# Kernel tuning notes

Measured on AMD Instinct MI355X. Metric: run time of the kernel, lower is better.

The kernel has to match this reference:

```python
import jax, jax.numpy as jnp
import numpy as np

N_HEADS = 16


def setup_inputs() -> dict:
    key = jax.random.key(0)
    ks = jax.random.split(key, 8)
    ts, td, b, hc = 64, 4096, 8, 1024
    scale = 1.0 / np.sqrt(hc)
    return {
        "s": jax.random.normal(ks[0], (ts, b, hc), dtype=jnp.float32),
        "d": jax.random.normal(ks[1], (td, b, hc), dtype=jnp.float32),
        "Wq": jax.random.normal(ks[2], (hc, hc), dtype=jnp.float32) * scale,
        "bq": jax.random.normal(ks[3], (hc,), dtype=jnp.float32) * 0.01,
        "Wk": jax.random.normal(ks[4], (hc, hc), dtype=jnp.float32) * scale,
        "bk": jax.random.normal(ks[5], (hc,), dtype=jnp.float32) * 0.01,
        "Wv": jax.random.normal(ks[6], (hc, hc), dtype=jnp.float32) * scale,
        "bv": jax.random.normal(ks[7], (hc,), dtype=jnp.float32) * 0.01,
    }


def reference(s, d, Wq, bq, Wk, bk, Wv, bv):
    ts, b, hc = s.shape
    td = d.shape[0]
    h = N_HEADS
    c = hc // h
    # linear projections (torch Linear: x @ W.T + b)
    q = (s @ Wq.T + bq).reshape(ts, b, h, c)
    k = (d @ Wk.T + bk).reshape(td, b, h, c)
    v = (d @ Wv.T + bv).reshape(td, b, h, c)
    # scores over (slot, token) pairs, scaled
    a = jnp.einsum('sbhc,dbhc->sdbh', q, k) / jnp.sqrt(jnp.asarray(c, s.dtype))
    # competitive softmax across the SLOT axis (dim 0), not the key axis
    a = jax.nn.softmax(a, axis=0)          # (ts, td, b, h)
    n = jnp.sum(a, axis=1) + 0.001         # (ts, b, h)
    num = jnp.einsum('sdbh,dbhc->sbhc', a, v)
    out = num / n[..., None]               # normalized weighted average
    return out.reshape(ts, b, hc)
```

## Files before the change

kernel.cpp:

```cpp
#include <hip/hip_runtime.h>


#define TS 64
#define TD 4096
#define BATCH 8
#define HC 1024
#define NHEAD 16
#define MD (TD*BATCH)
#define MS (TS*BATCH)
#define NCHUNK 8
#define CHTOK (TD/NCHUNK)

typedef __attribute__((ext_vector_type(8))) __bf16 bf16x8;
typedef __attribute__((ext_vector_type(4))) float f32x4;
typedef __attribute__((ext_vector_type(4))) unsigned short u16x4;
typedef __attribute__((ext_vector_type(8))) unsigned short u16x8;

__device__ __forceinline__ unsigned short f2bf(float x){
  union { float f; unsigned u; } v; v.f = x;
  unsigned r = v.u + 0x7FFFu + ((v.u >> 16) & 1u);
  return (unsigned short)(r >> 16);
}

__device__ __forceinline__ void gll16(const void* g, void* l){
  __builtin_amdgcn_global_load_lds((__attribute__((address_space(1))) void*)g,
                                   (__attribute__((address_space(3))) void*)l, 16, 0, 0);
}

__global__ void cvt_bf16(const float* __restrict__ in, unsigned short* __restrict__ out, int n4){
  int i = blockIdx.x * blockDim.x + threadIdx.x;
  if (i >= n4) return;
  f32x4 f = ((const f32x4*)in)[i];
  u16x4 o;
  o[0] = f2bf(f[0]); o[1] = f2bf(f[1]); o[2] = f2bf(f[2]); o[3] = f2bf(f[3]);
  ((u16x4*)out)[i] = o;
}

__global__ __launch_bounds__(256) void gemm128(
    const unsigned short* __restrict__ A,
    const unsigned short* __restrict__ W,
    const float* __restrict__ bias,
    unsigned short* __restrict__ C)
{
  __shared__ unsigned short As[128*64];
  __shared__ unsigned short Bs[128*64];
  const int nwg = gridDim.x;
  const int cpx = nwg >> 3;
  const int orig = blockIdx.x;
  const int wg = (orig & 7) * cpx + (orig >> 3);
  const int mt = wg >> 3, nt = wg & 7;
  const int tid = threadIdx.x;
  const int lane = tid & 63, w = tid >> 6;
  const int l15 = lane & 15, lg = lane >> 4;
  const int wr = w >> 1, wc = w & 1;

  const int lrow = lane >> 3;
  const int lch  = (lane & 7) << 4;
  const char* pA[4]; const char* pB[4]; unsigned ldsoff[4];
  #pragma unroll
  for (int j = 0; j < 4; ++j){
    int row = w*32 + j*8 + lrow;
    int sw  = lch ^ ((row & 7) << 4);
    pA[j] = (const char*)A + (size_t)(mt*128 + row) * 2048 + sw;
    pB[j] = (const char*)W + (size_t)(nt*128 + row) * 2048 + sw;
    ldsoff[j] = (unsigned)(w*32 + j*8) * 128;
  }

  const f32x4 fz = {0.f, 0.f, 0.f, 0.f};
  f32x4 acc[4][4];
  #pragma unroll
  for (int m = 0; m < 4; ++m)
    #pragma unroll
    for (int n = 0; n < 4; ++n) acc[m][n] = fz;

  for (int kt = 0; kt < 16; ++kt){
    __syncthreads();
    #pragma unroll
    for (int j = 0; j < 4; ++j){
      gll16(pA[j] + (size_t)kt*128, (char*)As + ldsoff[j]);
      gll16(pB[j] + (size_t)kt*128, (char*)Bs + ldsoff[j]);
    }
    __syncthreads();
    #pragma unroll
    for (int kk = 0; kk < 2; ++kk){
      bf16x8 af[4], bfr[4];
      #pragma unroll
      for (int m = 0; m < 4; ++m){
        int row = wr*64 + m*16 + l15;
        af[m] = *(const bf16x8*)((const char*)As + row*128 + ((lg*16 + kk*64) ^ ((row & 7) << 4)));
      }
      #pragma unroll
      for (int n = 0; n < 4; ++n){
        int row = wc*64 + n*16 + l15;
        bfr[n] = *(const bf16x8*)((const char*)Bs + row*128 + ((lg*16 + kk*64) ^ ((row & 7) << 4)));
      }
      #pragma unroll
      for (int m = 0; m < 4; ++m)
        #pragma unroll
        for (int n = 0; n < 4; ++n)
          acc[m][n] = __builtin_amdgcn_mfma_f32_16x16x32_bf16(af[m], bfr[n], acc[m][n], 0, 0, 0);
    }
  }

  const int ccol0 = nt*128 + wc*64;
  float bv[4];
  #pragma unroll
  for (int n = 0; n < 4; ++n) bv[n] = bias[ccol0 + n*16 + l15];
  #pragma unroll
  for (int m = 0; m < 4; ++m){
    #pragma unroll
    for (int r = 0; r < 4; ++r){
      size_t row = (size_t)(mt*128 + wr*64 + m*16 + lg*4 + r);
      unsigned short* cp = C + row*1024 + ccol0;
      #pragma unroll
      for (int n = 0; n < 4; ++n)
        cp[n*16 + l15] = f2bf(acc[m][n][r] + bv[n]);
    }
  }
}

__global__ __launch_bounds__(256) void attn_kernel(
    const unsigned short* __restrict__ Q,
    const unsigned short* __restrict__ K,
    const unsigned short* __restrict__ V,
    float* __restrict__ P)
{
  __shared__ unsigned short Qs[64*64];
  __shared__ unsigned short Ks[64*64];
  __shared__ unsigned short Vt[80*64];
  __shared__ unsigned short Al[64*64];
  __shared__ float red[256];

  const int bh = blockIdx.x;
  const int chunk = blockIdx.y;
  const int bb = bh >> 4, h = bh & 15;
  const int tid = threadIdx.x;
  const int lane = tid & 63, w = tid >> 6;
  const int l15 = lane & 15, lg = lane >> 4;
  const int lrow = lane >> 3, lch = (lane & 7) << 4;

  for (int i = tid; i < 16*64; i += 256){
    int r = i >> 6;
    Vt[(64 + r)*64 + (i & 63)] = (r == 0) ? (unsigned short)0x3F80 : (unsigned short)0;
  }

  #pragma unroll
  for (int j = 0; j < 2; ++j){
    int row = w*16 + j*8 + lrow;
    int sw = lch ^ ((row & 7) << 4);
    const char* g = (const char*)Q + (size_t)(row*BATCH + bb)*2048 + h*128 + sw;
    gll16(g, (char*)Qs + (w*16 + j*8)*128);
  }

  const f32x4 fz = {0.f, 0.f, 0.f, 0.f};
  f32x4 acc[5];
  #pragma unroll
  for (int nb = 0; nb < 5; ++nb) acc[nb] = fz;

  const int vtok = tid >> 2;
  const int vcg  = tid & 3;
  const int t0 = chunk * CHTOK;

  for (int tt = 0; tt < CHTOK/64; ++tt){
    const int tb = t0 + tt*64;
    #pragma unroll
    for (int j = 0; j < 2; ++j){
      int row = w*16 + j*8 + lrow;
      int sw = lch ^ ((row & 7) << 4);
      const char* g = (const char*)K + (size_t)((size_t)(tb + row)*BATCH + bb)*2048 + h*128 + sw;
      gll16(g, (char*)Ks + (w*16 + j*8)*128);
    }
    const char* vg = (const char*)V + (size_t)((size_t)(tb + vtok)*BATCH + bb)*2048 + h*128 + vcg*32;
    u16x8 v0 = *(const u16x8*)vg;
    u16x8 v1 = *(const u16x8*)(vg + 16);
    __syncthreads();

    bf16x8 qa[2];
    #pragma unroll
    for (int kk = 0; kk < 2; ++kk){
      int row = w*16 + l15;
      qa[kk] = *(const bf16x8*)((const char*)Qs + row*128 + ((lg*16 + kk*64) ^ ((row & 7) << 4)));
    }
    float e[4][4];
    #pragma unroll
    for (int nb = 0; nb < 4; ++nb){
      f32x4 s = fz;
      #pragma unroll
      for (int kk = 0; kk < 2; ++kk){
        int row = nb*16 + l15;
        bf16x8 kb = *(const bf16x8*)((const char*)Ks + row*128 + ((lg*16 + kk*64) ^ ((row & 7) << 4)));
        s = __builtin_amdgcn_mfma_f32_16x16x32_bf16(qa[kk], kb, s, 0, 0, 0);
      }
      #pragma unroll
      for (int r = 0; r < 4; ++r) e[nb][r] = __expf(s[r] * 0.125f);
    }
    #pragma unroll
    for (int nb = 0; nb < 4; ++nb){
      float cp = e[nb][0] + e[nb][1] + e[nb][2] + e[nb][3];
      cp += __shfl_xor(cp, 16);
      cp += __shfl_xor(cp, 32);
      if (lg == 0) red[w*64 + nb*16 + l15] = cp;
    }
    __syncthreads();

    #pragma unroll
    for (int nb = 0; nb < 4; ++nb){
      int col = nb*16 + l15;
      float dn = red[col] + red[64 + col] + red[128 + col] + red[192 + col];
      float inv = 1.0f / dn;
      #pragma unroll
      for (int r = 0; r < 4; ++r){
        int row = w*16 + lg*4 + r;
        Al[row*64 + ((((2*col)) ^ ((row & 7) << 4)) >> 1)] = f2bf(e[nb][r] * inv);
      }
    }
    #pragma unroll
    for (int ee = 0; ee < 8; ++ee){
      int c0 = vcg*16 + ee;
      int sw0 = (((c0 & 7) ^ (c0 >> 3)) & 7) << 4;
      Vt[c0*64 + (((2*vtok) ^ sw0) >> 1)] = v0[ee];
    }
    #pragma unroll
    for (int ee = 0; ee < 8; ++ee){
      int c1 = vcg*16 + 8 + ee;
      int sw1 = (((c1 & 7) ^ (c1 >> 3)) & 7) << 4;
      Vt[c1*64 + (((2*vtok) ^ sw1) >> 1)] = v1[ee];
    }
    __syncthreads();

    bf16x8 aa[2];
    #pragma unroll
    for (int kk = 0; kk < 2; ++kk){
      int row = w*16 + l15;
      aa[kk] = *(const bf16x8*)((const char*)Al + row*128 + ((lg*16 + kk*64) ^ ((row & 7) << 4)));
    }
    #pragma unroll
    for (int nb = 0; nb < 5; ++nb){
      #pragma unroll
      for (int kk = 0; kk < 2; ++kk){
        int row = nb*16 + l15;
        int sw = (((row & 7) ^ (row >> 3)) & 7) << 4;
        bf16x8 vb = *(const bf16x8*)((const char*)Vt + row*128 + ((lg*16 + kk*64) ^ sw));
        acc[nb] = __builtin_amdgcn_mfma_f32_16x16x32_bf16(aa[kk], vb, acc[nb], 0, 0, 0);
      }
    }
  }

  float* Pb = P + (size_t)(bh*NCHUNK + chunk) * 64 * 80;
  #pragma unroll
  for (int nb = 0; nb < 5; ++nb){
    #pragma unroll
    for (int r = 0; r < 4; ++r){
      int s = w*16 + lg*4 + r;
      Pb[(size_t)s*80 + nb*16 + l15] = acc[nb][r];
    }
  }
}

__global__ void reduce_out(const float* __restrict__ P, float* __restrict__ out){
  int flat = blockIdx.x * 256 + threadIdx.x;
  int c = flat & 63, s = (flat >> 6) & 63, bh = flat >> 12;
  int bb = bh >> 4, h = bh & 15;
  float sc = 0.f, sn = 0.f;
  #pragma unroll
  for (int ch = 0; ch < NCHUNK; ++ch){
    const float* base = P + ((size_t)(bh*NCHUNK + ch)*64 + s)*80;
    sc += base[c];
    sn += base[64];
  }
  out[((size_t)s*BATCH + bb)*1024 + h*64 + c] = sc / (sn + 0.001f);
}

extern "C" void kernel_launch(void* const* d_in, const int* in_sizes, int n_in,
                              void* d_out, int out_size, void* d_ws, size_t ws_size,
                              hipStream_t stream)
{
  const float* s  = (const float*)d_in[0];
  const float* d  = (const float*)d_in[1];
  const float* Wq = (const float*)d_in[2];
  const float* bq = (const float*)d_in[3];
  const float* Wk = (const float*)d_in[4];
  const float* bk = (const float*)d_in[5];
  const float* Wv = (const float*)d_in[6];
  const float* bv = (const float*)d_in[7];
  float* out = (float*)d_out;

  char* ws = (char*)d_ws;
  unsigned short* dbf = (unsigned short*)(ws);
  unsigned short* sbf = (unsigned short*)(ws + 67108864);
  unsigned short* wqb = (unsigned short*)(ws + 68157440);
  unsigned short* wkb = (unsigned short*)(ws + 70254592);
  unsigned short* wvb = (unsigned short*)(ws + 72351744);
  unsigned short* Qw  = (unsigned short*)(ws + 74448896);
  unsigned short* Kw  = (unsigned short*)(ws + 75497472);
  unsigned short* Vw  = (unsigned short*)(ws + 142606336);
  float*          Pw  = (float*)(ws + 209715200);

  (void)in_sizes; (void)n_in; (void)out_size; (void)ws_size;

  cvt_bf16<<<(MD*HC/4 + 255)/256, 256, 0, stream>>>(d,  dbf, MD*HC/4);
  cvt_bf16<<<(MS*HC/4 + 255)/256, 256, 0, stream>>>(s,  sbf, MS*HC/4);
  cvt_bf16<<<(HC*HC/4 + 255)/256, 256, 0, stream>>>(Wq, wqb, HC*HC/4);
  cvt_bf16<<<(HC*HC/4 + 255)/256, 256, 0, stream>>>(Wk, wkb, HC*HC/4);
  cvt_bf16<<<(HC*HC/4 + 255)/256, 256, 0, stream>>>(Wv, wvb, HC*HC/4);

  gemm128<<<(MS/128)*8, 256, 0, stream>>>(sbf, wqb, bq, Qw);
  gemm128<<<(MD/128)*8, 256, 0, stream>>>(dbf, wkb, bk, Kw);
  gemm128<<<(MD/128)*8, 256, 0, stream>>>(dbf, wvb, bv, Vw);

  attn_kernel<<<dim3(128, NCHUNK), 256, 0, stream>>>(Qw, Kw, Vw, Pw);

  reduce_out<<<(TS*BATCH*HC)/256, 256, 0, stream>>>(Pw, out);
}
```

Baseline: 272.5 us.

## Fuse K and V projections into one 256x256-tiled pipelined GEMM

Replaces the two separate 128-tile GEMM launches for the K and V projections with a single kernel. It treats the contiguous Wk and Wv bf16 buffers as one 2048-row weight matrix and picks the K or V output and bias by column tile. Each 512-thread block computes a 256x256 tile through a 4-stage LDS ring fed by global_load_lds, with interleaved barriers and setprio around the MFMA bursts. This raises operand reuse and overlaps loads with compute, but uses a lot of LDS and registers, which limits occupancy.

```diff
diff --git a/kernel.cpp b/kernel.cpp
--- a/kernel.cpp
+++ b/kernel.cpp
@@ -11,6 +11,8 @@
 #define NCHUNK 8
 #define CHTOK (TD/NCHUNK)
 
+#define KTILES 32
+
 typedef __attribute__((ext_vector_type(8))) __bf16 bf16x8;
 typedef __attribute__((ext_vector_type(4))) float f32x4;
 typedef __attribute__((ext_vector_type(4))) unsigned short u16x4;
@@ -34,6 +36,125 @@
   u16x4 o;
   o[0] = f2bf(f[0]); o[1] = f2bf(f[1]); o[2] = f2bf(f[2]); o[3] = f2bf(f[3]);
   ((u16x4*)out)[i] = o;
+}
+
+__global__ __launch_bounds__(512, 2) void gemm_kv(
+    const unsigned short* __restrict__ A,
+    const unsigned short* __restrict__ W,
+    const float* __restrict__ bk,
+    const float* __restrict__ bv,
+    unsigned short* __restrict__ Kout,
+    unsigned short* __restrict__ Vout)
+{
+  __shared__ unsigned short As[4][256*32];
+  __shared__ unsigned short Bs[4][256*32];
+
+  const int nwg = gridDim.x;
+  const int cpx = nwg >> 3;
+  const int orig = blockIdx.x;
+  const int wg = (orig & 7) * cpx + (orig >> 3);
+  const int mt = wg >> 3, nt = wg & 7;
+  const int tid = threadIdx.x;
+  const int lane = tid & 63, w = tid >> 6;
+  const int l15 = lane & 15, lg = lane >> 4;
+  const int wm = w >> 2, wn = w & 3;
+
+  const int lr = lane >> 2;
+  const int schunk = (((lane & 3) ^ ((lane >> 3) & 3)) << 4);
+  const char* pa[2]; const char* pb[2]; unsigned ldso[2];
+  #pragma unroll
+  for (int j = 0; j < 2; ++j){
+    int grow = j*128 + w*16 + lr;
+    pa[j] = (const char*)A + (size_t)(mt*256 + grow)*2048 + schunk;
+    pb[j] = (const char*)W + (size_t)(nt*256 + grow)*2048 + schunk;
+    ldso[j] = (unsigned)(j*8192 + w*1024);
+  }
+
+  #define STAGE_A(t) { char* d = (char*)&As[(t)&3][0]; \
+    gll16(pa[0] + (size_t)(t)*64, d + ldso[0]); \
+    gll16(pa[1] + (size_t)(t)*64, d + ldso[1]); }
+  #define STAGE_B(t) { char* d = (char*)&Bs[(t)&3][0]; \
+    gll16(pb[0] + (size_t)(t)*64, d + ldso[0]); \
+    gll16(pb[1] + (size_t)(t)*64, d + ldso[1]); }
+
+  const unsigned cswz = ((unsigned)(lg ^ ((l15 >> 1) & 3))) << 4;
+  const unsigned aoff = (unsigned)(wm*128 + l15)*64 + cswz;
+  const unsigned boff = (unsigned)(wn*64  + l15)*64 + cswz;
+
+  const f32x4 fz = {0.f, 0.f, 0.f, 0.f};
+  f32x4 acc[8][4];
+  #pragma unroll
+  for (int m = 0; m < 8; ++m)
+    #pragma unroll
+    for (int n = 0; n < 4; ++n) acc[m][n] = fz;
+
+  STAGE_A(0) STAGE_B(0) STAGE_A(1) STAGE_B(1) STAGE_A(2) STAGE_B(2)
+  asm volatile("s_waitcnt vmcnt(8)" ::: "memory");
+  __builtin_amdgcn_s_barrier();
+  __builtin_amdgcn_sched_barrier(0);
+
+  for (int t = 0; t < KTILES; ++t){
+    const char* as = (const char*)&As[t & 3][0];
+    const char* bs = (const char*)&Bs[t & 3][0];
+
+    bf16x8 af0[4], bfr[4];
+    #pragma unroll
+    for (int mf = 0; mf < 4; ++mf) af0[mf] = *(const bf16x8*)(as + aoff + mf*1024u);
+    #pragma unroll
+    for (int nf = 0; nf < 4; ++nf) bfr[nf] = *(const bf16x8*)(bs + boff + nf*1024u);
+    if (t + 3 < KTILES) STAGE_A(t + 3)
+    __builtin_amdgcn_s_barrier();
+    __builtin_amdgcn_sched_barrier(0);
+    __builtin_amdgcn_s_setprio(1);
+    #pragma unroll
+    for (int mf = 0; mf < 4; ++mf)
+      #pragma unroll
+      for (int nf = 0; nf < 4; ++nf)
+        acc[mf][nf] = __builtin_amdgcn_mfma_f32_16x16x32_bf16(af0[mf], bfr[nf], acc[mf][nf], 0, 0, 0);
+    __builtin_amdgcn_s_setprio(0);
+    __builtin_amdgcn_s_barrier();
+
+    bf16x8 af1[4];
+    #pragma unroll
+    for (int mf = 0; mf < 4; ++mf) af1[mf] = *(const bf16x8*)(as + aoff + (4 + mf)*1024u);
+    if (t + 3 < KTILES) STAGE_B(t + 3)
+    __builtin_amdgcn_s_barrier();
+    __builtin_amdgcn_sched_barrier(0);
+    __builtin_amdgcn_s_setprio(1);
+    #pragma unroll
+    for (int mf = 0; mf < 4; ++mf)
+      #pragma unroll
+      for (int nf = 0; nf < 4; ++nf)
+        acc[4 + mf][nf] = __builtin_amdgcn_mfma_f32_16x16x32_bf16(af1[mf], bfr[nf], acc[4 + mf][nf], 0, 0, 0);
+    __builtin_amdgcn_s_setprio(0);
+
+    __builtin_amdgcn_sched_barrier(0);
+    if (t < KTILES - 3)       { asm volatile("s_waitcnt vmcnt(8)" ::: "memory"); }
+    else if (t == KTILES - 3) { asm volatile("s_waitcnt vmcnt(4)" ::: "memory"); }
+    else if (t == KTILES - 2) { asm volatile("s_waitcnt vmcnt(0)" ::: "memory"); }
+    __builtin_amdgcn_s_barrier();
+    __builtin_amdgcn_sched_barrier(0);
+  }
+
+  const int ccol = (nt & 3)*256 + wn*64;
+  unsigned short* Cb = (nt < 4) ? Kout : Vout;
+  const float* bias = (nt < 4) ? bk : bv;
+  float bvv[4];
+  #pragma unroll
+  for (int nf = 0; nf < 4; ++nf) bvv[nf] = bias[ccol + nf*16 + l15];
+  #pragma unroll
+  for (int mf = 0; mf < 8; ++mf){
+    #pragma unroll
+    for (int r = 0; r < 4; ++r){
+      size_t row = (size_t)(mt*256 + wm*128 + mf*16 + lg*4 + r);
+      unsigned short* cp = Cb + row*1024 + ccol;
+      #pragma unroll
+      for (int nf = 0; nf < 4; ++nf)
+        cp[nf*16 + l15] = f2bf(acc[mf][nf][r] + bvv[nf]);
+    }
+  }
+  #undef STAGE_A
+  #undef STAGE_B
 }
 
 __global__ __launch_bounds__(256) void gemm128(
@@ -305,8 +426,7 @@
   cvt_bf16<<<(HC*HC/4 + 255)/256, 256, 0, stream>>>(Wv, wvb, HC*HC/4);
 
   gemm128<<<(MS/128)*8, 256, 0, stream>>>(sbf, wqb, bq, Qw);
-  gemm128<<<(MD/128)*8, 256, 0, stream>>>(dbf, wkb, bk, Kw);
-  gemm128<<<(MD/128)*8, 256, 0, stream>>>(dbf, wvb, bv, Vw);
+  gemm_kv<<<(MD/256)*8, 512, 0, stream>>>(dbf, wkb, bk, bv, Kw, Vw);
 
   attn_kernel<<<dim3(128, NCHUNK), 256, 0, stream>>>(Qw, Kw, Vw, Pw);
 
```

New measurement: 256.0 us. 6.1% less time.

## Fuse K/V projections into one 256x256-tile GEMM and merge conversion launches

Applied to the files above, without the earlier changes.

Merges the five fp32-to-bf16 conversion launches into one kernel that dispatches on the global index. Replaces the separate K and V projection GEMMs with a single GEMM over the concatenated Wk/Wv weights (N=2048), using 256x256 tiles, 512 threads, double-buffered LDS with direct global-to-LDS loads, and a hand-scheduled waitcnt/barrier pipeline. This reads the activations d once instead of twice, raises arithmetic intensity per tile, and cuts launch overhead. The cost is heavy LDS use (128KB), high register pressure from 32 accumulators per thread, and fragile manual vmcnt accounting.

```diff
diff --git a/kernel.cpp b/kernel.cpp
--- a/kernel.cpp
+++ b/kernel.cpp
@@ -27,13 +27,227 @@
                                    (__attribute__((address_space(3))) void*)l, 16, 0, 0);
 }
 
-__global__ void cvt_bf16(const float* __restrict__ in, unsigned short* __restrict__ out, int n4){
-  int i = blockIdx.x * blockDim.x + threadIdx.x;
-  if (i >= n4) return;
-  f32x4 f = ((const f32x4*)in)[i];
+__global__ void cvt_all(const float* __restrict__ d, const float* __restrict__ s,
+                        const float* __restrict__ wq, const float* __restrict__ wk,
+                        const float* __restrict__ wv,
+                        unsigned short* __restrict__ dbf, unsigned short* __restrict__ sbf,
+                        unsigned short* __restrict__ wqb, unsigned short* __restrict__ wkb,
+                        unsigned short* __restrict__ wvb){
+  long i = (long)blockIdx.x * 256 + threadIdx.x;
+  const float* src; unsigned short* dst; long off;
+  if (i < 8388608L)      { src = d;  dst = dbf; off = i; }
+  else if (i < 8519680L) { src = s;  dst = sbf; off = i - 8388608L; }
+  else if (i < 8781824L) { src = wq; dst = wqb; off = i - 8519680L; }
+  else if (i < 9043968L) { src = wk; dst = wkb; off = i - 8781824L; }
+  else                   { src = wv; dst = wvb; off = i - 9043968L; }
+  f32x4 f = ((const f32x4*)src)[off];
   u16x4 o;
   o[0] = f2bf(f[0]); o[1] = f2bf(f[1]); o[2] = f2bf(f[2]); o[3] = f2bf(f[3]);
-  ((u16x4*)out)[i] = o;
+  ((u16x4*)dst)[off] = o;
+}
+
+__global__ __launch_bounds__(512, 2) void gemm_kv(
+    const unsigned short* __restrict__ A,
+    const unsigned short* __restrict__ W,
+    const float* __restrict__ bk,
+    const float* __restrict__ bv,
+    unsigned short* __restrict__ Kout,
+    unsigned short* __restrict__ Vout)
+{
+  __shared__ unsigned short As[2][256*64];
+  __shared__ unsigned short Bs[2][256*64];
+
+  const int nwg = gridDim.x;
+  const int cpx = nwg >> 3;
+  const int orig = blockIdx.x;
+  const int wg = (orig & 7) * cpx + (orig >> 3);
+  const int mt = wg >> 3, nt = wg & 7;
+  const int tid = threadIdx.x;
+  const int lane = tid & 63, w = tid >> 6;
+  const int l15 = lane & 15, lg = lane >> 4;
+  const int wm = w >> 2, wn = w & 3;
+
+  const int lr8 = lane >> 3;
+  const unsigned sch8 = (unsigned)((lane & 7) ^ lr8) << 4;
+  const char* aBase = (const char*)A + (size_t)mt * 256 * 2048;
+  const char* bBase = (const char*)W + (size_t)nt * 256 * 2048;
+  unsigned rowbyte[4]; unsigned ldsg[4];
+  #pragma unroll
+  for (int g = 0; g < 4; ++g){
+    rowbyte[g] = (unsigned)((g*64 + w*8 + lr8) * 2048) + sch8;
+    ldsg[g]    = (unsigned)((g*64 + w*8) * 128);
+  }
+
+  #define SA(kt_, g_, buf_) { if ((kt_) < 16) gll16(aBase + rowbyte[g_] + (size_t)(kt_)*128, (char*)&As[buf_][0] + ldsg[g_]); }
+  #define SB(kt_, g_, buf_) { if ((kt_) < 16) gll16(bBase + rowbyte[g_] + (size_t)(kt_)*128, (char*)&Bs[buf_][0] + ldsg[g_]); }
+
+  const unsigned arow = (unsigned)(wm*128 + l15) * 128;
+  const unsigned brow = (unsigned)(wn*64  + l15) * 128;
+  const unsigned ck0 = (unsigned)((lg      ^ (l15 & 7)) << 4);
+  const unsigned ck1 = (unsigned)(((4+lg)  ^ (l15 & 7)) << 4);
+
+  #define RD_A(buf_, mf_, kk_) (*(const bf16x8*)((const char*)&As[buf_][0] + arow + (mf_)*2048u + ((kk_) ? ck1 : ck0)))
+  #define RD_B(buf_, nf_, kk_) (*(const bf16x8*)((const char*)&Bs[buf_][0] + brow + (nf_)*2048u + ((kk_) ? ck1 : ck0)))
+
+  const f32x4 fz = {0.f, 0.f, 0.f, 0.f};
+  f32x4 acc[8][4];
+  #pragma unroll
+  for (int m = 0; m < 8; ++m)
+    #pragma unroll
+    for (int n = 0; n < 4; ++n) acc[m][n] = fz;
+
+  #define MMQ(q_) { \
+    __builtin_amdgcn_s_setprio(1); \
+    _Pragma("unroll") \
+    for (int kk = 0; kk < 2; ++kk){ \
+      _Pragma("unroll") \
+      for (int nf = 0; nf < 4; ++nf){ \
+        acc[2*(q_)  ][nf] = __builtin_amdgcn_mfma_f32_16x16x32_bf16(af[0][kk], bfr[nf][kk], acc[2*(q_)  ][nf], 0,0,0); \
+        acc[2*(q_)+1][nf] = __builtin_amdgcn_mfma_f32_16x16x32_bf16(af[1][kk], bfr[nf][kk], acc[2*(q_)+1][nf], 0,0,0); \
+      } } \
+    __builtin_amdgcn_s_setprio(0); }
+
+  #define BAR       { __builtin_amdgcn_s_barrier(); __builtin_amdgcn_sched_barrier(0); }
+  #define LGKM0     { asm volatile("s_waitcnt lgkmcnt(0)" ::: "memory"); __builtin_amdgcn_sched_barrier(0); }
+  #define LGKM8     { asm volatile("s_waitcnt lgkmcnt(8)" ::: "memory"); __builtin_amdgcn_sched_barrier(0); }
+
+  SA(0,0,0) SA(0,1,0) SA(0,2,0) SA(0,3,0)
+  SB(0,0,0) SB(0,1,0) SB(0,2,0) SB(0,3,0)
+  SB(1,0,1) SB(1,1,1) SB(1,2,1) SB(1,3,1)
+  SA(1,0,1) SA(1,2,1)
+  asm volatile("s_waitcnt vmcnt(6)" ::: "memory");
+  __builtin_amdgcn_sched_barrier(0);
+  BAR
+
+  #pragma unroll 1
+  for (int i = 0; i < 8; ++i){
+    const int kodd = 2*i + 1, s2 = 2*i + 2, s3 = 2*i + 3;
+    bf16x8 bfr[4][2];
+
+    {
+      bf16x8 af[2][2];
+      #pragma unroll
+      for (int nf = 0; nf < 4; ++nf){ bfr[nf][0] = RD_B(0, nf, 0); bfr[nf][1] = RD_B(0, nf, 1); }
+      af[0][0] = RD_A(0, 0, 0); af[0][1] = RD_A(0, 0, 1);
+      af[1][0] = RD_A(0, 1, 0); af[1][1] = RD_A(0, 1, 1);
+      SA(kodd, 1, 1) SA(kodd, 3, 1)
+      LGKM8
+      BAR
+      LGKM0
+      MMQ(0)
+      BAR
+    }
+    {
+      bf16x8 af[2][2];
+      af[0][0] = RD_A(0, 2, 0); af[0][1] = RD_A(0, 2, 1);
+      af[1][0] = RD_A(0, 3, 0); af[1][1] = RD_A(0, 3, 1);
+      SB(s2, 0, 0) SB(s2, 1, 0)
+      BAR
+      LGKM0
+      MMQ(1)
+      BAR
+    }
+    {
+      bf16x8 af[2][2];
+      af[0][0] = RD_A(0, 4, 0); af[0][1] = RD_A(0, 4, 1);
+      af[1][0] = RD_A(0, 5, 0); af[1][1] = RD_A(0, 5, 1);
+      SA(s2, 0, 0) SA(s2, 2, 0)
+      BAR
+      LGKM0
+      MMQ(2)
+      BAR
+    }
+    {
+      bf16x8 af[2][2];
+      af[0][0] = RD_A(0, 6, 0); af[0][1] = RD_A(0, 6, 1);
+      af[1][0] = RD_A(0, 7, 0); af[1][1] = RD_A(0, 7, 1);
+      SB(s2, 2, 0) SB(s2, 3, 0)
+      BAR
+      LGKM0
+      MMQ(3)
+      __builtin_amdgcn_sched_barrier(0);
+      if (i < 7) { asm volatile("s_waitcnt vmcnt(8)" ::: "memory"); }
+      else       { asm volatile("s_waitcnt vmcnt(2)" ::: "memory"); }
+      __builtin_amdgcn_sched_barrier(0);
+      BAR
+    }
+    {
+      bf16x8 af[2][2];
+      #pragma unroll
+      for (int nf = 0; nf < 4; ++nf){ bfr[nf][0] = RD_B(1, nf, 0); bfr[nf][1] = RD_B(1, nf, 1); }
+      af[0][0] = RD_A(1, 0, 0); af[0][1] = RD_A(1, 0, 1);
+      af[1][0] = RD_A(1, 1, 0); af[1][1] = RD_A(1, 1, 1);
+      SA(s2, 1, 0) SA(s2, 3, 0)
+      LGKM8
+      BAR
+      LGKM0
+      MMQ(0)
+      BAR
+    }
+    {
+      bf16x8 af[2][2];
+      af[0][0] = RD_A(1, 2, 0); af[0][1] = RD_A(1, 2, 1);
+      af[1][0] = RD_A(1, 3, 0); af[1][1] = RD_A(1, 3, 1);
+      SB(s3, 0, 1) SB(s3, 1, 1)
+      BAR
+      LGKM0
+      MMQ(1)
+      __builtin_amdgcn_sched_barrier(0);
+      if (i < 7) { asm volatile("s_waitcnt vmcnt(10)" ::: "memory"); }
+      else       { asm volatile("s_waitcnt vmcnt(0)" ::: "memory"); }
+      __builtin_amdgcn_sched_barrier(0);
+      BAR
+    }
+    {
+      bf16x8 af[2][2];
+      af[0][0] = RD_A(1, 4, 0); af[0][1] = RD_A(1, 4, 1);
+      af[1][0] = RD_A(1, 5, 0); af[1][1] = RD_A(1, 5, 1);
+      SA(s3, 0, 1) SA(s3, 2, 1)
+      BAR
+      LGKM0
+      MMQ(2)
+      BAR
+    }
+    {
+      bf16x8 af[2][2];
+      af[0][0] = RD_A(1, 6, 0); af[0][1] = RD_A(1, 6, 1);
+      af[1][0] = RD_A(1, 7, 0); af[1][1] = RD_A(1, 7, 1);
+      SB(s3, 2, 1) SB(s3, 3, 1)
+      BAR
+      LGKM0
+      MMQ(3)
+      __builtin_amdgcn_sched_barrier(0);
+      if (i < 7) { asm volatile("s_waitcnt vmcnt(6)" ::: "memory"); }
+      __builtin_amdgcn_sched_barrier(0);
+      BAR
+    }
+  }
+
+  const int ccol = (nt & 3)*256 + wn*64;
+  unsigned short* Cb = (nt < 4) ? Kout : Vout;
+  const float* bias = (nt < 4) ? bk : bv;
+  float bvv[4];
+  #pragma unroll
+  for (int nf = 0; nf < 4; ++nf) bvv[nf] = bias[ccol + nf*16 + l15];
+  #pragma unroll
+  for (int mf = 0; mf < 8; ++mf){
+    #pragma unroll
+    for (int r = 0; r < 4; ++r){
+      size_t row = (size_t)(mt*256 + wm*128 + mf*16 + lg*4 + r);
+      unsigned short* cp = Cb + row*1024 + ccol;
+      #pragma unroll
+      for (int nf = 0; nf < 4; ++nf)
+        cp[nf*16 + l15] = f2bf(acc[mf][nf][r] + bvv[nf]);
+    }
+  }
+  #undef SA
+  #undef SB
+  #undef RD_A
+  #undef RD_B
+  #undef MMQ
+  #undef BAR
+  #undef LGKM0
+  #undef LGKM8
 }
 
 __global__ __launch_bounds__(256) void gemm128(
@@ -298,15 +512,10 @@
 
   (void)in_sizes; (void)n_in; (void)out_size; (void)ws_size;
 
-  cvt_bf16<<<(MD*HC/4 + 255)/256, 256, 0, stream>>>(d,  dbf, MD*HC/4);
-  cvt_bf16<<<(MS*HC/4 + 255)/256, 256, 0, stream>>>(s,  sbf, MS*HC/4);
-  cvt_bf16<<<(HC*HC/4 + 255)/256, 256, 0, stream>>>(Wq, wqb, HC*HC/4);
-  cvt_bf16<<<(HC*HC/4 + 255)/256, 256, 0, stream>>>(Wk, wkb, HC*HC/4);
-  cvt_bf16<<<(HC*HC/4 + 255)/256, 256, 0, stream>>>(Wv, wvb, HC*HC/4);
+  cvt_all<<<36352, 256, 0, stream>>>(d, s, Wq, Wk, Wv, dbf, sbf, wqb, wkb, wvb);
 
   gemm128<<<(MS/128)*8, 256, 0, stream>>>(sbf, wqb, bq, Qw);
-  gemm128<<<(MD/128)*8, 256, 0, stream>>>(dbf, wkb, bk, Kw);
-  gemm128<<<(MD/128)*8, 256, 0, stream>>>(dbf, wvb, bv, Vw);
+  gemm_kv<<<(MD/256)*8, 512, 0, stream>>>(dbf, wkb, bk, bv, Kw, Vw);
 
   attn_kernel<<<dim3(128, NCHUNK), 256, 0, stream>>>(Qw, Kw, Vw, Pw);
 
```

Result: faster. 241.2 us (-11.5%).

## Fuse K/V projections into one double-buffered GEMM and merge conversion launches

Applied to the files above, without the earlier changes.

The five float-to-bf16 conversion launches become a single kernel that picks its source and destination buffer by global index range. The separate K and V projection GEMMs are replaced by one gemm_kv kernel using 256x128 tiles with double-buffered LDS staging. It treats the contiguous Wk/Wv bf16 buffers as one 2048-row weight matrix and sends the output to K or V by column tile. The aim is to cut launch overhead, reuse each d tile across both projections, and overlap global-to-LDS loads with MFMA work. In exchange it relies on Wk and Wv sitting next to each other in the workspace and uses larger per-thread accumulator state.

```diff
diff --git a/kernel.cpp b/kernel.cpp
--- a/kernel.cpp
+++ b/kernel.cpp
@@ -27,13 +27,130 @@
                                    (__attribute__((address_space(3))) void*)l, 16, 0, 0);
 }
 
-__global__ void cvt_bf16(const float* __restrict__ in, unsigned short* __restrict__ out, int n4){
-  int i = blockIdx.x * blockDim.x + threadIdx.x;
-  if (i >= n4) return;
-  f32x4 f = ((const f32x4*)in)[i];
+__global__ void cvt_all(const float* __restrict__ d, const float* __restrict__ s,
+                        const float* __restrict__ wq, const float* __restrict__ wk,
+                        const float* __restrict__ wv,
+                        unsigned short* __restrict__ dbf, unsigned short* __restrict__ sbf,
+                        unsigned short* __restrict__ wqb, unsigned short* __restrict__ wkb,
+                        unsigned short* __restrict__ wvb){
+  long i = (long)blockIdx.x * 256 + threadIdx.x;
+  const float* src; unsigned short* dst; long off;
+  if (i < 8388608L)      { src = d;  dst = dbf; off = i; }
+  else if (i < 8519680L) { src = s;  dst = sbf; off = i - 8388608L; }
+  else if (i < 8781824L) { src = wq; dst = wqb; off = i - 8519680L; }
+  else if (i < 9043968L) { src = wk; dst = wkb; off = i - 8781824L; }
+  else                   { src = wv; dst = wvb; off = i - 9043968L; }
+  f32x4 f = ((const f32x4*)src)[off];
   u16x4 o;
   o[0] = f2bf(f[0]); o[1] = f2bf(f[1]); o[2] = f2bf(f[2]); o[3] = f2bf(f[3]);
-  ((u16x4*)out)[i] = o;
+  ((u16x4*)dst)[off] = o;
+}
+
+__global__ __launch_bounds__(256, 2) void gemm_kv(
+    const unsigned short* __restrict__ A,
+    const unsigned short* __restrict__ W,
+    const float* __restrict__ bk,
+    const float* __restrict__ bv,
+    unsigned short* __restrict__ Kout,
+    unsigned short* __restrict__ Vout)
+{
+  __shared__ unsigned short As[2][256*32];
+  __shared__ unsigned short Bs[2][128*32];
+
+  const int nwg = gridDim.x;
+  const int cpx = nwg >> 3;
+  const int orig = blockIdx.x;
+  const int wg = (orig & 7) * cpx + (orig >> 3);
+  const int mt = wg >> 4, nt = wg & 15;
+  const int tid = threadIdx.x;
+  const int lane = tid & 63, w = tid >> 6;
+  const int l15 = lane & 15, lg = lane >> 4;
+  const int wm = w >> 1, wn = w & 1;
+
+  const int srow = lane >> 2;
+  const unsigned schunk = (unsigned)(((lane & 3) ^ ((lane >> 3) & 3)) << 4);
+  const char* aS = (const char*)A + (size_t)(mt*256) * 2048 + schunk;
+  const char* bS = (const char*)W + (size_t)(nt*128) * 2048 + schunk;
+  const unsigned ar0 = (unsigned)((  0 + w*16 + srow) * 2048);
+  const unsigned ar1 = (unsigned)(( 64 + w*16 + srow) * 2048);
+  const unsigned ar2 = (unsigned)((128 + w*16 + srow) * 2048);
+  const unsigned ar3 = (unsigned)((192 + w*16 + srow) * 2048);
+  const unsigned br0 = ar0, br1 = ar1;
+  const unsigned da0 = (unsigned)((  0 + w*16) * 64);
+  const unsigned da1 = (unsigned)(( 64 + w*16) * 64);
+  const unsigned da2 = (unsigned)((128 + w*16) * 64);
+  const unsigned da3 = (unsigned)((192 + w*16) * 64);
+
+  #define STAGE(t_, buf_) { \
+    const size_t ko = (size_t)(t_) * 64; \
+    char* dA = (char*)&As[buf_][0]; char* dB = (char*)&Bs[buf_][0]; \
+    gll16(aS + ar0 + ko, dA + da0); \
+    gll16(aS + ar1 + ko, dA + da1); \
+    gll16(aS + ar2 + ko, dA + da2); \
+    gll16(aS + ar3 + ko, dA + da3); \
+    gll16(bS + br0 + ko, dB + da0); \
+    gll16(bS + br1 + ko, dB + da1); \
+    __builtin_amdgcn_sched_barrier(0); }
+
+  const unsigned ksel = (unsigned)((lg ^ ((l15 >> 1) & 3)) << 4);
+  const unsigned aoff = (unsigned)(wm*128 + l15) * 64 + ksel;
+  const unsigned boff = (unsigned)(wn*64  + l15) * 64 + ksel;
+
+  const f32x4 fz = {0.f, 0.f, 0.f, 0.f};
+  f32x4 acc[8][4];
+  #pragma unroll
+  for (int m = 0; m < 8; ++m)
+    #pragma unroll
+    for (int n = 0; n < 4; ++n) acc[m][n] = fz;
+
+  #define TILE(buf_) { \
+    const char* as_ = (const char*)&As[buf_][0]; \
+    const char* bs_ = (const char*)&Bs[buf_][0]; \
+    bf16x8 af[8], bf[4]; \
+    _Pragma("unroll") \
+    for (int m = 0; m < 8; ++m) af[m] = *(const bf16x8*)(as_ + aoff + m*1024u); \
+    _Pragma("unroll") \
+    for (int n = 0; n < 4; ++n) bf[n] = *(const bf16x8*)(bs_ + boff + n*1024u); \
+    __builtin_amdgcn_s_setprio(1); \
+    _Pragma("unroll") \
+    for (int m = 0; m < 8; ++m) \
+      _Pragma("unroll") \
+      for (int n = 0; n < 4; ++n) \
+        acc[m][n] = __builtin_amdgcn_mfma_f32_16x16x32_bf16(af[m], bf[n], acc[m][n], 0, 0, 0); \
+    __builtin_amdgcn_s_setprio(0); }
+
+  STAGE(0, 0)
+  __syncthreads();
+
+  #pragma unroll 1
+  for (int tp = 0; tp < 16; ++tp){
+    STAGE(2*tp + 1, 1)
+    TILE(0)
+    __syncthreads();
+    if (tp < 15) STAGE(2*tp + 2, 0)
+    TILE(1)
+    __syncthreads();
+  }
+
+  const int ccol = (nt & 7)*128 + wn*64;
+  unsigned short* Cb = (nt < 8) ? Kout : Vout;
+  const float* bias = (nt < 8) ? bk : bv;
+  float bvv[4];
+  #pragma unroll
+  for (int nf = 0; nf < 4; ++nf) bvv[nf] = bias[ccol + nf*16 + l15];
+  #pragma unroll
+  for (int mf = 0; mf < 8; ++mf){
+    #pragma unroll
+    for (int r = 0; r < 4; ++r){
+      size_t row = (size_t)(mt*256 + wm*128 + mf*16 + lg*4 + r);
+      unsigned short* cp = Cb + row*1024 + ccol;
+      #pragma unroll
+      for (int nf = 0; nf < 4; ++nf)
+        cp[nf*16 + l15] = f2bf(acc[mf][nf][r] + bvv[nf]);
+    }
+  }
+  #undef STAGE
+  #undef TILE
 }
 
 __global__ __launch_bounds__(256) void gemm128(
@@ -298,15 +415,10 @@
 
   (void)in_sizes; (void)n_in; (void)out_size; (void)ws_size;
 
-  cvt_bf16<<<(MD*HC/4 + 255)/256, 256, 0, stream>>>(d,  dbf, MD*HC/4);
-  cvt_bf16<<<(MS*HC/4 + 255)/256, 256, 0, stream>>>(s,  sbf, MS*HC/4);
-  cvt_bf16<<<(HC*HC/4 + 255)/256, 256, 0, stream>>>(Wq, wqb, HC*HC/4);
-  cvt_bf16<<<(HC*HC/4 + 255)/256, 256, 0, stream>>>(Wk, wkb, HC*HC/4);
-  cvt_bf16<<<(HC*HC/4 + 255)/256, 256, 0, stream>>>(Wv, wvb, HC*HC/4);
+  cvt_all<<<36352, 256, 0, stream>>>(d, s, Wq, Wk, Wv, dbf, sbf, wqb, wkb, wvb);
 
   gemm128<<<(MS/128)*8, 256, 0, stream>>>(sbf, wqb, bq, Qw);
-  gemm128<<<(MD/128)*8, 256, 0, stream>>>(dbf, wkb, bk, Kw);
-  gemm128<<<(MD/128)*8, 256, 0, stream>>>(dbf, wvb, bv, Vw);
+  gemm_kv<<<(MD/256)*16, 256, 0, stream>>>(dbf, wkb, bk, bv, Kw, Vw);
 
   attn_kernel<<<dim3(128, NCHUNK), 256, 0, stream>>>(Qw, Kw, Vw, Pw);
 
```

After: 254.4 us. -6.6%, faster.
